# Performance work log

Hardware: AMD Instinct MI355X
Metric: run time of the kernel (lower is better)

Reference implementation:

```python
import jax, jax.numpy as jnp
import numpy as np

IN_CHANNELS = 8
CHANNELS = 8
MASK_OUT_STRIDE = 4


def aligned_bilinear(x, factor):
    # Faithful port of AdelaiDet aligned_bilinear (align_corners=True).
    if factor == 1:
        return x
    n, c, h, w = x.shape
    x = jnp.pad(x, ((0, 0), (0, 0), (0, 1), (0, 1)), mode='edge')
    oh, ow = factor * h + 1, factor * w + 1

    def interp_axis(arr, out_len, axis):
        # align_corners=True from size s+1 -> factor*s+1: src coord = i / factor
        coords = jnp.arange(out_len) / factor
        i0 = jnp.floor(coords).astype(jnp.int32)
        i1 = jnp.minimum(i0 + 1, arr.shape[axis] - 1)
        t = (coords - i0).astype(arr.dtype)
        a0 = jnp.take(arr, i0, axis=axis)
        a1 = jnp.take(arr, i1, axis=axis)
        shp = [1] * arr.ndim
        shp[axis] = out_len
        t = t.reshape(shp)
        return a0 * (1 - t) + a1 * t

    x = interp_axis(x, oh, 2)
    x = interp_axis(x, ow, 3)
    p = factor // 2
    x = jnp.pad(x, ((0, 0), (0, 0), (p, 0), (p, 0)), mode='edge')
    return x[:, :, : oh - 1, : ow - 1]


def setup_inputs() -> dict:
    key = jax.random.key(0)
    ks = jax.random.split(key, 6)
    N, C, H, W = 4, IN_CHANNELS, 112, 200
    n_inst = 200
    stride = 8
    num_gen_params = (C + 2) * CHANNELS + CHANNELS + CHANNELS * CHANNELS + CHANNELS + CHANNELS + 1  # 169
    mask_feats = jax.random.normal(ks[0], (N, C, H, W), dtype=jnp.float32)
    mask_head_params = jax.random.normal(ks[1], (n_inst, num_gen_params), dtype=jnp.float32) * 0.1
    # instance centers anywhere inside the image (in input-image pixel coords)
    instance_locations = jax.random.uniform(ks[2], (n_inst, 2), dtype=jnp.float32) * jnp.array(
        [W * stride, H * stride], dtype=jnp.float32)
    sizes_of_interest = jnp.array([64.0, 128.0, 256.0, 512.0, 1024.0], dtype=jnp.float32)
    im_inds = jax.random.randint(ks[3], (n_inst,), 0, N, dtype=jnp.int32)
    fpn_levels = jax.random.randint(ks[4], (n_inst,), 0, 5, dtype=jnp.int32)
    return {
        'mask_feats': mask_feats,
        'mask_head_params': mask_head_params,
        'instance_locations': instance_locations,
        'sizes_of_interest': sizes_of_interest,
        'im_inds': im_inds,
        'fpn_levels': fpn_levels,
        'mask_feat_stride': stride,
    }


def reference(mask_feats, mask_head_params, instance_locations, sizes_of_interest,
              im_inds, fpn_levels, mask_feat_stride):
    N, C, H, W = mask_feats.shape
    n_inst = mask_head_params.shape[0]
    HW = H * W
    stride = mask_feat_stride  # python int

    # compute_locations: (x, y) pairs, x fastest, at pixel centers (stride//2 offset)
    xs = (jnp.arange(W) * stride + stride // 2).astype(mask_feats.dtype)
    ys = (jnp.arange(H) * stride + stride // 2).astype(mask_feats.dtype)
    gx, gy = jnp.meshgrid(xs, ys, indexing='xy')  # [H, W]
    locations = jnp.stack([gx, gy], axis=-1).reshape(HW, 2)  # [HW, 2]

    # relative coords, normalized by size-of-interest per instance
    rel = instance_locations[:, None, :] - locations[None, :, :]  # [n, HW, 2]
    rel = jnp.transpose(rel, (0, 2, 1))  # [n, 2, HW]
    soi = sizes_of_interest[fpn_levels]  # [n]
    rel = rel / soi[:, None, None]

    feats = mask_feats[im_inds].reshape(n_inst, C, HW)  # [n, C, HW]
    x = jnp.concatenate([rel, feats], axis=1)  # [n, C+2, HW]

    # parse_dynamic_params: split [n, 169] into per-layer 1x1 conv weights/biases
    wn = [(C + 2) * CHANNELS, CHANNELS * CHANNELS, CHANNELS * 1]
    bn = [CHANNELS, CHANNELS, 1]
    sizes = wn + bn
    offs = np.cumsum([0] + sizes)
    parts = [mask_head_params[:, offs[i]:offs[i + 1]] for i in range(len(sizes))]
    w0 = parts[0].reshape(n_inst, CHANNELS, C + 2)
    w1 = parts[1].reshape(n_inst, CHANNELS, CHANNELS)
    w2 = parts[2].reshape(n_inst, 1, CHANNELS)
    b0, b1, b2 = parts[3], parts[4], parts[5]

    # per-instance grouped 1x1 convs == batched matmuls over instances
    x = jax.nn.relu(jnp.einsum('noi,nip->nop', w0, x) + b0[:, :, None])
    x = jax.nn.relu(jnp.einsum('noi,nip->nop', w1, x) + b1[:, :, None])
    x = jnp.einsum('noi,nip->nop', w2, x) + b2[:, :, None]  # [n, 1, HW]

    mask_logits = x.reshape(n_inst, 1, H, W)
    factor = stride // MASK_OUT_STRIDE
    return aligned_bilinear(mask_logits, factor)
```

## Files before the change

### kernel.cpp

```cpp
#include <hip/hip_runtime.h>


#define IN_C   8
#define CHN    8
#define Hh     112
#define Ww     200
#define HWp    (Hh * Ww)
#define OH     224
#define OW     400
#define TY     16
#define RL     9
#define NPIX   (RL * Ww)
#define NTILES (OH / TY)
#define NPARAMS 169
#define BLK    256


__global__ __launch_bounds__(BLK, 4)
void dmh_fused_kernel(const float* __restrict__ feats,
                      const float* __restrict__ params,
                      const float* __restrict__ iloc,
                      const float* __restrict__ soi_tab,
                      const int*   __restrict__ im_inds,
                      const int*   __restrict__ fpn_levels,
                      float* __restrict__ out)
{
    __shared__ float lgt[RL][Ww];

    const int bid  = blockIdx.x;
    const int inst = bid / NTILES;
    const int ty   = bid - inst * NTILES;
    const int y0   = ty * TY;
    const int r_lo = (y0 > 0 ? (y0 - 1) : 0) >> 1;
    const int tid  = threadIdx.x;

    const float* __restrict__ wp = params + inst * NPARAMS;
    const float soi    = soi_tab[fpn_levels[inst]];
    const float inv_s  = 1.0f / soi;
    const float ix     = iloc[inst * 2 + 0];
    const float iy     = iloc[inst * 2 + 1];
    const float* __restrict__ fb = feats + (size_t)im_inds[inst] * (IN_C * HWp);

    float w0s[80];
    #pragma unroll
    for (int i = 0; i < 80; i++) w0s[i] = wp[i];
    #pragma unroll
    for (int i = 0; i < 80; i++) asm volatile("" : "+s"(w0s[i]));

    float w1v[64], w2v[CHN], b0v[CHN], b1v[CHN], b2v;
    #pragma unroll
    for (int i = 0; i < 64; i++) w1v[i] = wp[80 + i];
    #pragma unroll
    for (int i = 0; i < CHN; i++) w2v[i] = wp[144 + i];
    #pragma unroll
    for (int i = 0; i < CHN; i++) b0v[i] = wp[152 + i];
    #pragma unroll
    for (int i = 0; i < CHN; i++) b1v[i] = wp[160 + i];
    b2v = wp[168];
    #pragma unroll
    for (int i = 0; i < 64; i++) asm volatile("" : "+v"(w1v[i]));
    #pragma unroll
    for (int i = 0; i < CHN; i++) asm volatile("" : "+v"(w2v[i]));
    #pragma unroll
    for (int i = 0; i < CHN; i++) asm volatile("" : "+v"(b0v[i]));
    #pragma unroll
    for (int i = 0; i < CHN; i++) asm volatile("" : "+v"(b1v[i]));
    asm volatile("" : "+v"(b2v));

    for (int g = tid; g < NPIX; g += BLK) {
        const int rr = g / Ww;
        const int c  = g - rr * Ww;
        const int r  = r_lo + rr;
        const float* fp = fb + r * Ww + c;

        float fv[IN_C];
        #pragma unroll
        for (int ch = 0; ch < IN_C; ch++) fv[ch] = fp[ch * HWp];

        const float in1 = (iy - (float)(r * 8 + 4)) * inv_s;
        const float in0 = (ix - (float)(c * 8 + 4)) * inv_s;

        float h1a[CHN];
        #pragma unroll
        for (int o = 0; o < CHN; o++) h1a[o] = b1v[o];

        #pragma unroll
        for (int o = 0; o < CHN; o++) {
            float t = fmaf(w0s[o * 10 + 1], in1, b0v[o]);
            t = fmaf(w0s[o * 10 + 0], in0, t);
            #pragma unroll
            for (int i = 0; i < IN_C; i++)
                t = fmaf(w0s[o * 10 + 2 + i], fv[i], t);
            t = fmaxf(t, 0.0f);
            #pragma unroll
            for (int oo = 0; oo < CHN; oo++)
                h1a[oo] = fmaf(w1v[oo * 8 + o], t, h1a[oo]);
        }
        float r0 = b2v;
        #pragma unroll
        for (int i = 0; i < CHN; i++)
            r0 = fmaf(w2v[i], fmaxf(h1a[i], 0.0f), r0);

        lgt[rr][c] = r0;
    }
    __syncthreads();

    float* __restrict__ ob = out + (size_t)inst * (OH * OW);
    const int NQ = (TY * OW) / 4;
    for (int q = tid; q < NQ; q += BLK) {
        const int dy = q / (OW / 4);
        const int gx = q - dy * (OW / 4);
        const int x  = gx * 4;
        const int y  = y0 + dy;
        const int i  = (y > 0 ? y - 1 : 0);
        const int rr0 = (i >> 1) - r_lo;
        const int r1g = (i >> 1) + (i & 1);
        const int rr1 = (r1g > Hh - 1 ? Hh - 1 : r1g) - r_lo;
        const float wy1 = (i & 1) ? 0.5f : 0.0f;
        const float wy0 = 1.0f - wy1;

        const int cx  = x >> 1;
        const int cm1 = (cx > 0 ? cx - 1 : 0);
        const float a_m = lgt[rr0][cm1], a_0 = lgt[rr0][cx], a_p = lgt[rr0][cx + 1];
        const float b_m = lgt[rr1][cm1], b_0 = lgt[rr1][cx], b_p = lgt[rr1][cx + 1];
        const float Rm = wy0 * a_m + wy1 * b_m;
        const float R0 = wy0 * a_0 + wy1 * b_0;
        const float Rp = wy0 * a_p + wy1 * b_p;

        float4 o4;
        o4.x = 0.5f * (Rm + R0);
        o4.y = R0;
        o4.z = 0.5f * (R0 + Rp);
        o4.w = Rp;
        *reinterpret_cast<float4*>(&ob[y * OW + x]) = o4;
    }
}

extern "C" void kernel_launch(void* const* d_in, const int* in_sizes, int n_in,
                              void* d_out, int out_size, void* d_ws, size_t ws_size,
                              hipStream_t stream) {
    const float* mask_feats = (const float*)d_in[0];
    const float* params     = (const float*)d_in[1];
    const float* iloc       = (const float*)d_in[2];
    const float* soi        = (const float*)d_in[3];
    const int*   im_inds    = (const int*)d_in[4];
    const int*   fpn        = (const int*)d_in[5];
    float* out = (float*)d_out;

    const int n_inst = in_sizes[4];
    dim3 grid(n_inst * NTILES);
    dim3 block(BLK);
    hipLaunchKernelGGL(dmh_fused_kernel, grid, block, 0, stream,
                       mask_feats, params, iloc, soi, im_inds, fpn, out);
}
```

Measured before the change: 39.96 us.

## Use packed fp16 dot2 for the per-pixel MLP with weights in scalar registers

Converts the dynamic conv weights, input features and intermediate activations to packed fp16 pairs and evaluates all three 1x1 layers with v_dot2_f32_f16, accumulating in fp32. All weights are made wave-uniform via readfirstlane and held in SGPRs, and the biases are staged in shared memory. This frees the 64+ VGPRs previously used for w1, so launch bounds rise to 8 waves per SIMD, and it roughly halves the ALU instruction count of the MLP. The cost is reduced precision in the inputs, weights and hidden activations, which may exceed the tolerance, plus an extra syncthreads.

Result: slower. 48.02 us (+20.2%).

```diff
diff --git a/kernel.cpp b/kernel.cpp
--- a/kernel.cpp
+++ b/kernel.cpp
@@ -15,8 +15,25 @@
 #define NPARAMS 169
 #define BLK    256
 
-
-__global__ __launch_bounds__(BLK, 4)
+typedef __fp16 h2v __attribute__((ext_vector_type(2)));
+
+__device__ __forceinline__ uint pkh(float a, float b) {
+    h2v p = __builtin_amdgcn_cvt_pkrtz(a, b);
+    union { h2v v; uint u; } cv; cv.v = p; return cv.u;
+}
+__device__ __forceinline__ float fdot2u(uint a, uint b, float c) {
+    union { uint u; h2v v; } ua, ub; ua.u = a; ub.u = b;
+#if __has_builtin(__builtin_amdgcn_fdot2)
+    return __builtin_amdgcn_fdot2(ua.v, ub.v, c, false);
+#else
+    float d;
+    asm("v_dot2_f32_f16 %0, %1, %2, %3" : "=v"(d) : "v"(ua.v), "v"(ub.v), "v"(c));
+    return d;
+#endif
+}
+
+
+__global__ __launch_bounds__(BLK, 8)
 void dmh_fused_kernel(const float* __restrict__ feats,
                       const float* __restrict__ params,
                       const float* __restrict__ iloc,
@@ -25,6 +42,7 @@
                       const int*   __restrict__ fpn_levels,
                       float* __restrict__ out)
 {
+    __shared__ float bl[20];
     __shared__ float lgt[RL][Ww];
 
     const int bid  = blockIdx.x;
@@ -35,71 +53,100 @@
     const int tid  = threadIdx.x;
 
     const float* __restrict__ wp = params + inst * NPARAMS;
+    if (tid < 8)       bl[tid]      = wp[152 + tid];
+    else if (tid < 16) bl[tid]      = wp[160 + (tid - 8)];
+    else if (tid == 16) bl[16]      = wp[168];
+
+    uint w0p[40], w1p[32], w2p[4];
+    #pragma unroll
+    for (int o = 0; o < CHN; o++) {
+        w0p[o * 5 + 0] = pkh(wp[o * 10 + 0], wp[o * 10 + 1]);
+        #pragma unroll
+        for (int j = 0; j < 4; j++)
+            w0p[o * 5 + 1 + j] = pkh(wp[o * 10 + 2 + 2 * j], wp[o * 10 + 3 + 2 * j]);
+    }
+    #pragma unroll
+    for (int o = 0; o < CHN; o++)
+        #pragma unroll
+        for (int j = 0; j < 4; j++)
+            w1p[o * 4 + j] = pkh(wp[80 + o * 8 + 2 * j], wp[80 + o * 8 + 2 * j + 1]);
+    #pragma unroll
+    for (int j = 0; j < 4; j++)
+        w2p[j] = pkh(wp[144 + 2 * j], wp[144 + 2 * j + 1]);
+
+    #pragma unroll
+    for (int i = 0; i < 40; i++) {
+        w0p[i] = __builtin_amdgcn_readfirstlane(w0p[i]);
+        asm volatile("" : "+s"(w0p[i]));
+    }
+    #pragma unroll
+    for (int i = 0; i < 32; i++) {
+        w1p[i] = __builtin_amdgcn_readfirstlane(w1p[i]);
+        asm volatile("" : "+s"(w1p[i]));
+    }
+    #pragma unroll
+    for (int i = 0; i < 4; i++) {
+        w2p[i] = __builtin_amdgcn_readfirstlane(w2p[i]);
+        asm volatile("" : "+s"(w2p[i]));
+    }
+
     const float soi    = soi_tab[fpn_levels[inst]];
     const float inv_s  = 1.0f / soi;
     const float ix     = iloc[inst * 2 + 0];
     const float iy     = iloc[inst * 2 + 1];
     const float* __restrict__ fb = feats + (size_t)im_inds[inst] * (IN_C * HWp);
 
-    float w0s[80];
-    #pragma unroll
-    for (int i = 0; i < 80; i++) w0s[i] = wp[i];
-    #pragma unroll
-    for (int i = 0; i < 80; i++) asm volatile("" : "+s"(w0s[i]));
-
-    float w1v[64], w2v[CHN], b0v[CHN], b1v[CHN], b2v;
-    #pragma unroll
-    for (int i = 0; i < 64; i++) w1v[i] = wp[80 + i];
-    #pragma unroll
-    for (int i = 0; i < CHN; i++) w2v[i] = wp[144 + i];
-    #pragma unroll
-    for (int i = 0; i < CHN; i++) b0v[i] = wp[152 + i];
-    #pragma unroll
-    for (int i = 0; i < CHN; i++) b1v[i] = wp[160 + i];
-    b2v = wp[168];
-    #pragma unroll
-    for (int i = 0; i < 64; i++) asm volatile("" : "+v"(w1v[i]));
-    #pragma unroll
-    for (int i = 0; i < CHN; i++) asm volatile("" : "+v"(w2v[i]));
-    #pragma unroll
-    for (int i = 0; i < CHN; i++) asm volatile("" : "+v"(b0v[i]));
-    #pragma unroll
-    for (int i = 0; i < CHN; i++) asm volatile("" : "+v"(b1v[i]));
-    asm volatile("" : "+v"(b2v));
-
-    for (int g = tid; g < NPIX; g += BLK) {
-        const int rr = g / Ww;
-        const int c  = g - rr * Ww;
+    __syncthreads();
+
+    for (int p = tid; p < NPIX; p += BLK) {
+        const int rr = p / Ww;
+        const int c  = p - rr * Ww;
         const int r  = r_lo + rr;
         const float* fp = fb + r * Ww + c;
 
-        float fv[IN_C];
-        #pragma unroll
-        for (int ch = 0; ch < IN_C; ch++) fv[ch] = fp[ch * HWp];
+        uint f_pk[4];
+        #pragma unroll
+        for (int j = 0; j < 4; j++)
+            f_pk[j] = pkh(fp[(2 * j) * HWp], fp[(2 * j + 1) * HWp]);
 
         const float in1 = (iy - (float)(r * 8 + 4)) * inv_s;
         const float in0 = (ix - (float)(c * 8 + 4)) * inv_s;
-
-        float h1a[CHN];
-        #pragma unroll
-        for (int o = 0; o < CHN; o++) h1a[o] = b1v[o];
-
+        const uint  in_pk = pkh(in0, in1);
+
+        float hv[CHN];
         #pragma unroll
         for (int o = 0; o < CHN; o++) {
-            float t = fmaf(w0s[o * 10 + 1], in1, b0v[o]);
-            t = fmaf(w0s[o * 10 + 0], in0, t);
-            #pragma unroll
-            for (int i = 0; i < IN_C; i++)
-                t = fmaf(w0s[o * 10 + 2 + i], fv[i], t);
-            t = fmaxf(t, 0.0f);
-            #pragma unroll
-            for (int oo = 0; oo < CHN; oo++)
-                h1a[oo] = fmaf(w1v[oo * 8 + o], t, h1a[oo]);
+            float t = bl[o];
+            t = fdot2u(in_pk,  w0p[o * 5 + 0], t);
+            t = fdot2u(f_pk[0], w0p[o * 5 + 1], t);
+            t = fdot2u(f_pk[1], w0p[o * 5 + 2], t);
+            t = fdot2u(f_pk[2], w0p[o * 5 + 3], t);
+            t = fdot2u(f_pk[3], w0p[o * 5 + 4], t);
+            hv[o] = fmaxf(t, 0.0f);
         }
-        float r0 = b2v;
-        #pragma unroll
-        for (int i = 0; i < CHN; i++)
-            r0 = fmaf(w2v[i], fmaxf(h1a[i], 0.0f), r0);
+        uint h_pk[4];
+        #pragma unroll
+        for (int j = 0; j < 4; j++) h_pk[j] = pkh(hv[2 * j], hv[2 * j + 1]);
+
+        float gv[CHN];
+        #pragma unroll
+        for (int o = 0; o < CHN; o++) {
+            float a = bl[8 + o];
+            a = fdot2u(h_pk[0], w1p[o * 4 + 0], a);
+            a = fdot2u(h_pk[1], w1p[o * 4 + 1], a);
+            a = fdot2u(h_pk[2], w1p[o * 4 + 2], a);
+            a = fdot2u(h_pk[3], w1p[o * 4 + 3], a);
+            gv[o] = fmaxf(a, 0.0f);
+        }
+        uint g_pk[4];
+        #pragma unroll
+        for (int j = 0; j < 4; j++) g_pk[j] = pkh(gv[2 * j], gv[2 * j + 1]);
+
+        float r0 = bl[16];
+        r0 = fdot2u(g_pk[0], w2p[0], r0);
+        r0 = fdot2u(g_pk[1], w2p[1], r0);
+        r0 = fdot2u(g_pk[2], w2p[2], r0);
+        r0 = fdot2u(g_pk[3], w2p[3], r0);
 
         lgt[rr][c] = r0;
     }
```
